# Kernel optimization log

Measured on AMD Instinct MI355X. Metric: run time of the kernel, lower is better.

The kernel has to match this reference:

```python
import jax, jax.numpy as jnp
import numpy as np

B, N, D, H, F = 2, 2048, 512, 8, 2048
HD = D // H
EPS = 1e-5

def _ln(x, g, b):
    m = jnp.mean(x, axis=-1, keepdims=True)
    v = jnp.mean((x - m) ** 2, axis=-1, keepdims=True)
    return (x - m) * jax.lax.rsqrt(v + EPS) * g + b

def setup_inputs() -> dict:
    key = jax.random.key(0)
    ks = jax.random.split(key, 20)
    def lin(k, din, dout, std=0.05):
        kw, kb = jax.random.split(k)
        return (jax.random.normal(kw, (din, dout), jnp.float32) * std,
                jnp.zeros((dout,), jnp.float32))
    Wq, bq = lin(ks[0], D, D)
    Wk, bk = lin(ks[1], D, D)
    Wv, bv = lin(ks[2], D, D)
    Wg, bg = lin(ks[3], D, D)
    Wo, bo = lin(ks[4], D, D)
    W1, b1 = lin(ks[5], D, F)
    W2, b2 = lin(ks[6], F, D)
    return {
        'x': jax.random.normal(ks[7], (B, N, D), jnp.float32),
        'attn_bias': jax.random.normal(ks[8], (B, N, N, H), jnp.float32) * 0.1,
        'attn_mask': jnp.zeros((B, N, N), jnp.bool_),
        'Wq': Wq, 'bq': bq, 'Wk': Wk, 'bk': bk, 'Wv': Wv, 'bv': bv,
        'Wg': Wg, 'bg': bg, 'Wo': Wo, 'bo': bo,
        'ln1_g': jnp.ones((D,), jnp.float32), 'ln1_b': jnp.zeros((D,), jnp.float32),
        'ln2_g': jnp.ones((D,), jnp.float32), 'ln2_b': jnp.zeros((D,), jnp.float32),
        'W1': W1, 'b1': b1, 'W2': W2, 'b2': b2,
    }

def reference(x, attn_bias, attn_mask, Wq, bq, Wk, bk, Wv, bv, Wg, bg, Wo, bo,
              ln1_g, ln1_b, ln2_g, ln2_b, W1, b1, W2, b2):
    scaling = HD ** -0.5
    # --- self-attention sublayer (pre-LN) ---
    y = _ln(x, ln1_g, ln1_b)
    q = (y @ Wq + bq).reshape(B, N, H, HD) * scaling
    k = (y @ Wk + bk).reshape(B, N, H, HD)
    v = (y @ Wv + bv).reshape(B, N, H, HD)
    u = y * jax.nn.sigmoid(y @ Wg + bg)            # GLU gating branch
    scores = jnp.einsum('bqhd,bkhd->bqkh', q, k)   # [B, Nq, Nk, H]
    scores = scores + attn_bias                    # attn_bias_type == 'add'
    scores = jnp.where(attn_mask[..., None], -jnp.inf, scores)
    w = jax.nn.softmax(scores, axis=2)             # softmax over keys
    attn = jnp.einsum('bqkh,bkhd->bqhd', w, v).reshape(B, N, D)
    attn = attn @ Wo + bo
    y = u + attn
    x = x + y                                      # residual (dropout = identity, eval)
    # --- FFN sublayer (pre-LN) ---
    y = _ln(x, ln2_g, ln2_b)
    y = jax.nn.gelu(y @ W1 + b1, approximate=False) @ W2 + b2
    return x + y
```

## Files before the change

### kernel.cpp

```cpp
#include <hip/hip_runtime.h>
#include <hip/hip_bf16.h>

#define DI __device__ __forceinline__

typedef __attribute__((ext_vector_type(8))) __bf16 bf16x8;
typedef __attribute__((ext_vector_type(4))) float f32x4;
typedef __attribute__((ext_vector_type(4))) unsigned short u16x4;
typedef __attribute__((ext_vector_type(8))) unsigned short u16x8;

DI unsigned short f2bs(float f) {
  __hip_bfloat16 h = __float2bfloat16(f);
  return __builtin_bit_cast(unsigned short, h);
}
DI float bs2f(unsigned short s) {
  return __bfloat162float(__builtin_bit_cast(__hip_bfloat16, s));
}
DI f32x4 mfma16(bf16x8 a, bf16x8 b, f32x4 c) {
  return __builtin_amdgcn_mfma_f32_16x16x32_bf16(a, b, c, 0, 0, 0);
}
DI void g2lds16(const void* g, void* l) {
  __builtin_amdgcn_global_load_lds(
      (__attribute__((address_space(1))) void*)(unsigned long long)g,
      (__attribute__((address_space(3))) void*)l, 16, 0, 0);
}
DI void block_sync_lds() {
  asm volatile("s_waitcnt lgkmcnt(0)" ::: "memory");
  __builtin_amdgcn_sched_barrier(0);
  __builtin_amdgcn_s_barrier();
  __builtin_amdgcn_sched_barrier(0);
}

__global__ __launch_bounds__(256) void k_transw(const float* __restrict__ W,
                                                unsigned short* __restrict__ Wt,
                                                int K, int N) {
  __shared__ float tile[64][65];
  int tk = blockIdx.x * 64, tn = blockIdx.y * 64;
  int t = threadIdx.x;
#pragma unroll
  for (int i = 0; i < 16; ++i) {
    int idx = t + i * 256;
    int r = idx >> 6, c = idx & 63;
    tile[r][c] = W[(size_t)(tk + r) * N + tn + c];
  }
  __syncthreads();
#pragma unroll
  for (int i = 0; i < 16; ++i) {
    int idx = t + i * 256;
    int n = idx >> 6, kk = idx & 63;
    Wt[(size_t)(tn + n) * K + tk + kk] = f2bs(tile[kk][n]);
  }
}

__global__ __launch_bounds__(256) void k_bcat(const float* __restrict__ bq,
                                              const float* __restrict__ bk,
                                              const float* __restrict__ bv,
                                              const float* __restrict__ bg,
                                              float* __restrict__ bcat) {
  int t = blockIdx.x * 256 + threadIdx.x;
  const float* src = t < 512 ? bq : t < 1024 ? bk : t < 1536 ? bv : bg;
  bcat[t] = src[t & 511];
}

__global__ __launch_bounds__(256) void k_ln(const float* __restrict__ x,
                                            const float* __restrict__ g,
                                            const float* __restrict__ b,
                                            unsigned short* __restrict__ y) {
  int row = blockIdx.x, t = threadIdx.x;
  const float* xr = x + (size_t)row * 512;
  float a0 = xr[t], a1 = xr[t + 256];
  float s1 = a0 + a1, s2 = a0 * a0 + a1 * a1;
#pragma unroll
  for (int o = 32; o > 0; o >>= 1) {
    s1 += __shfl_down(s1, o);
    s2 += __shfl_down(s2, o);
  }
  __shared__ float r1[4], r2[4], bc[2];
  int w = t >> 6, l = t & 63;
  if (l == 0) { r1[w] = s1; r2[w] = s2; }
  __syncthreads();
  if (t == 0) {
    float t1 = r1[0] + r1[1] + r1[2] + r1[3];
    float t2 = r2[0] + r2[1] + r2[2] + r2[3];
    float m = t1 / 512.f;
    float v = t2 / 512.f - m * m;
    bc[0] = m;
    bc[1] = rsqrtf(v + 1e-5f);
  }
  __syncthreads();
  float m = bc[0], inv = bc[1];
  y[(size_t)row * 512 + t] = f2bs((a0 - m) * inv * g[t] + b[t]);
  y[(size_t)row * 512 + t + 256] = f2bs((a1 - m) * inv * g[t + 256] + b[t + 256]);
}

template <int BM>
__global__ __launch_bounds__(256) void k_gemm(
    const unsigned short* __restrict__ A, const unsigned short* __restrict__ Bt,
    const float* __restrict__ bias, int M, int N, int K, int mode,
    float* __restrict__ outf, unsigned short* __restrict__ outh,
    const float* __restrict__ add1, const float* __restrict__ add2,
    unsigned short* __restrict__ vtout) {
  constexpr int MI = BM / 32;
  __shared__ __align__(16) unsigned short lA[BM * 64];
  __shared__ __align__(16) unsigned short lB[64 * 64];
  int t = threadIdx.x, w = t >> 6, l = t & 63;
  int l15 = l & 15, lg = l >> 4;
  int m0 = blockIdx.x * BM, n0 = blockIdx.y * 64;
  int wm = (w >> 1) * (BM / 2), wn = (w & 1) * 32;
  f32x4 acc[MI][2] = {};
  int sr = l >> 3, scb = (l & 7) * 16;
  for (int k0 = 0; k0 < K; k0 += 64) {
#pragma unroll
    for (int c = 0; c < MI; ++c) {
      int row = w * (BM / 4) + sr + c * 8;
      g2lds16((const char*)A + ((size_t)(m0 + row) * K + k0) * 2 + scb,
              (char*)lA + w * (BM / 4) * 128 + c * 1024);
    }
#pragma unroll
    for (int c = 0; c < 2; ++c) {
      int row = w * 16 + sr + c * 8;
      g2lds16((const char*)Bt + ((size_t)(n0 + row) * K + k0) * 2 + scb,
              (char*)lB + w * 2048 + c * 1024);
    }
    __syncthreads();
#pragma unroll
    for (int kc = 0; kc < 2; ++kc) {
      bf16x8 af[MI], bfr[2];
#pragma unroll
      for (int i = 0; i < MI; ++i)
        af[i] = *(const bf16x8*)((const char*)lA + (wm + i * 16 + l15) * 128 + kc * 64 + lg * 16);
#pragma unroll
      for (int j = 0; j < 2; ++j)
        bfr[j] = *(const bf16x8*)((const char*)lB + (wn + j * 16 + l15) * 128 + kc * 64 + lg * 16);
#pragma unroll
      for (int i = 0; i < MI; ++i)
#pragma unroll
        for (int j = 0; j < 2; ++j)
          acc[i][j] = mfma16(af[i], bfr[j], acc[i][j]);
    }
    __syncthreads();
  }
#pragma unroll
  for (int i = 0; i < MI; ++i) {
#pragma unroll
    for (int j = 0; j < 2; ++j) {
      int col = n0 + wn + j * 16 + l15;
      int row0 = m0 + wm + i * 16 + lg * 4;
      float vals[4];
#pragma unroll
      for (int r = 0; r < 4; ++r) vals[r] = acc[i][j][r] + bias[col];
      if (mode == 6) {
        int sel = col >> 9, c5 = col & 511;
        if (sel == 2) {
          int hh = c5 >> 6, dd = c5 & 63, bb = row0 >> 11, nn = row0 & 2047;
          u16x4 pk;
#pragma unroll
          for (int r = 0; r < 4; ++r) pk[r] = f2bs(vals[r]);
          *(u16x4*)(vtout + (((size_t)(bb * 8 + hh) * 64 + dd) * 2048 + nn)) = pk;
        } else {
#pragma unroll
          for (int r = 0; r < 4; ++r) {
            size_t idx = (size_t)(row0 + r) * 512 + c5;
            if (sel == 0) outh[idx] = f2bs(vals[r] * 0.125f);
            else if (sel == 1) outh[2097152 + idx] = f2bs(vals[r]);
            else outf[idx] = bs2f(A[idx]) * (1.f / (1.f + __expf(-vals[r])));
          }
        }
      } else {
#pragma unroll
        for (int r = 0; r < 4; ++r) {
          size_t idx = (size_t)(row0 + r) * N + col;
          if (mode == 3) outf[idx] = vals[r] + add1[idx] + add2[idx];
          else if (mode == 4) outh[idx] = f2bs(0.5f * vals[r] * (1.f + erff(vals[r] * 0.70710678f)));
          else outf[idx] = vals[r] + add1[idx];
        }
      }
    }
  }
}

__global__ __launch_bounds__(512, 1) void k_attn8(
    const unsigned short* __restrict__ q, const unsigned short* __restrict__ kk,
    const unsigned short* __restrict__ vt, const float* __restrict__ bias,
    const unsigned char* __restrict__ mask, unsigned short* __restrict__ ao) {
  __shared__ __align__(16) unsigned short lsB[2][16 * 260];
  __shared__ __align__(16) unsigned short ls_p[8][16][36];

  int bid = blockIdx.x;
  int b = bid & 1, qt = bid >> 1;
  int q0 = qt * 16;
  int t = threadIdx.x, w = t >> 6, l = t & 63;
  int l15 = l & 15, lg = l >> 4;
  int h = w;

  bf16x8 qa0 = *(const bf16x8*)(q + ((size_t)(b * 2048 + q0 + l15) * 512 + h * 64 + lg * 8));
  bf16x8 qa1 = *(const bf16x8*)(q + ((size_t)(b * 2048 + q0 + l15) * 512 + h * 64 + 32 + lg * 8));

  union { bf16x8 v; unsigned short s[8]; } uo;
#pragma unroll
  for (int j = 0; j < 8; ++j) uo.s[j] = 0x3F80;
  const bf16x8 vones = uo.v;

  f32x4 oacc[4] = {};
  f32x4 lacc = {};

  const unsigned short* kbase = kk + ((size_t)(b * 2048) + l15) * 512 + h * 64 + lg * 8;
  const unsigned short* vbase = vt + ((size_t)(b * 8 + h) * 64 + l15) * 2048 + lg * 8;

  int qq = t >> 5, kc = t & 31;
  const float* bptr = bias + ((size_t)(b * 2048 + q0 + qq) * 2048 + kc) * 8;
  const unsigned char* mptr = mask + (size_t)(b * 2048 + q0 + qq) * 2048 + kc;
  const unsigned short BN = f2bs(-1e30f);

#define LOADB(BA, BB, MB, kb)                                                \
  do {                                                                       \
    BA = *(const float4*)(bptr + (size_t)(kb) * 8);                          \
    BB = *(const float4*)(bptr + (size_t)(kb) * 8 + 4);                      \
    MB = mptr[kb];                                                           \
  } while (0)
#define WRITEB(buf, BA, BB, MB)                                              \
  do {                                                                       \
    u16x4 o0, o1;                                                            \
    if (MB) {                                                                \
      o0[0] = o0[1] = o0[2] = o0[3] = BN;                                    \
      o1[0] = o1[1] = o1[2] = o1[3] = BN;                                    \
    } else {                                                                 \
      o0[0] = f2bs(BA.x); o0[1] = f2bs(BA.y); o0[2] = f2bs(BA.z);            \
      o0[3] = f2bs(BA.w); o1[0] = f2bs(BB.x); o1[1] = f2bs(BB.y);            \
      o1[2] = f2bs(BB.z); o1[3] = f2bs(BB.w);                                \
    }                                                                        \
    *(u16x4*)&lsB[buf][qq * 260 + kc * 8] = o0;                              \
    *(u16x4*)&lsB[buf][qq * 260 + kc * 8 + 4] = o1;                          \
  } while (0)
#define COMPUTE(buf, kb)                                                     \
  do {                                                                       \
    const unsigned short* kp = kbase + (size_t)(kb)*512;                     \
    bf16x8 k00 = *(const bf16x8*)(kp);                                       \
    bf16x8 k01 = *(const bf16x8*)(kp + 32);                                  \
    bf16x8 k10 = *(const bf16x8*)(kp + 16 * 512);                            \
    bf16x8 k11 = *(const bf16x8*)(kp + 16 * 512 + 32);                       \
    const unsigned short* vp = vbase + (kb);                                 \
    bf16x8 v0 = *(const bf16x8*)(vp);                                        \
    bf16x8 v1 = *(const bf16x8*)(vp + 16 * 2048);                            \
    bf16x8 v2 = *(const bf16x8*)(vp + 32 * 2048);                            \
    bf16x8 v3 = *(const bf16x8*)(vp + 48 * 2048);                            \
    f32x4 sc0 = {}, sc1 = {};                                                \
    sc0 = mfma16(qa0, k00, sc0);                                             \
    sc0 = mfma16(qa1, k01, sc0);                                             \
    sc1 = mfma16(qa0, k10, sc1);                                             \
    sc1 = mfma16(qa1, k11, sc1);                                             \
    _Pragma("unroll") for (int r = 0; r < 4; ++r) {                          \
      int qr = lg * 4 + r;                                                   \
      float b0 = bs2f(lsB[buf][qr * 260 + l15 * 8 + h]);                     \
      float b1 = bs2f(lsB[buf][qr * 260 + (l15 + 16) * 8 + h]);              \
      float p0 = __expf(sc0[r] + b0 - 8.0f);                                 \
      float p1 = __expf(sc1[r] + b1 - 8.0f);                                 \
      ls_p[w][qr][l15] = f2bs(p0);                                           \
      ls_p[w][qr][16 + l15] = f2bs(p1);                                      \
    }                                                                        \
    bf16x8 pa = *(const bf16x8*)&ls_p[w][l15][lg * 8];                       \
    oacc[0] = mfma16(pa, v0, oacc[0]);                                       \
    oacc[1] = mfma16(pa, v1, oacc[1]);                                       \
    oacc[2] = mfma16(pa, v2, oacc[2]);                                       \
    oacc[3] = mfma16(pa, v3, oacc[3]);                                       \
    lacc = mfma16(pa, vones, lacc);                                          \
  } while (0)

  float4 bA0, bA1, bB0, bB1;
  unsigned char mA, mB;
  LOADB(bA0, bA1, mA, 0);
  WRITEB(0, bA0, bA1, mA);
  LOADB(bB0, bB1, mB, 32);
  block_sync_lds();
  for (int it = 0; it < 64; it += 2) {
    int kb2 = (it + 2 < 64) ? (it + 2) * 32 : 0;
    LOADB(bA0, bA1, mA, kb2);
    COMPUTE(0, it * 32);
    WRITEB(1, bB0, bB1, mB);
    block_sync_lds();
    int kb3 = (it + 3 < 64) ? (it + 3) * 32 : 0;
    LOADB(bB0, bB1, mB, kb3);
    COMPUTE(1, (it + 1) * 32);
    WRITEB(0, bA0, bA1, mA);
    block_sync_lds();
  }
#undef LOADB
#undef WRITEB
#undef COMPUTE

#pragma unroll
  for (int d = 0; d < 4; ++d)
#pragma unroll
    for (int r = 0; r < 4; ++r) {
      size_t row = (size_t)(b * 2048 + q0 + lg * 4 + r);
      ao[row * 512 + h * 64 + d * 16 + l15] = f2bs(oacc[d][r] / lacc[r]);
    }
}

extern "C" void kernel_launch(void* const* d_in, const int* in_sizes, int n_in,
                              void* d_out, int out_size, void* d_ws, size_t ws_size,
                              hipStream_t stream) {
  (void)in_sizes; (void)n_in; (void)out_size; (void)ws_size;
  const float* x = (const float*)d_in[0];
  const float* abias = (const float*)d_in[1];
  const unsigned char* amask = (const unsigned char*)d_in[2];
  const float* Wq = (const float*)d_in[3];
  const float* bq = (const float*)d_in[4];
  const float* Wk = (const float*)d_in[5];
  const float* bk = (const float*)d_in[6];
  const float* Wv = (const float*)d_in[7];
  const float* bv = (const float*)d_in[8];
  const float* Wg = (const float*)d_in[9];
  const float* bg = (const float*)d_in[10];
  const float* Wo = (const float*)d_in[11];
  const float* bo = (const float*)d_in[12];
  const float* ln1g = (const float*)d_in[13];
  const float* ln1b = (const float*)d_in[14];
  const float* ln2g = (const float*)d_in[15];
  const float* ln2b = (const float*)d_in[16];
  const float* W1 = (const float*)d_in[17];
  const float* b1 = (const float*)d_in[18];
  const float* W2 = (const float*)d_in[19];
  const float* b2 = (const float*)d_in[20];
  float* outp = (float*)d_out;

  char* ws = (char*)d_ws;
  const size_t MB = 1024 * 1024;

  unsigned short* qb = (unsigned short*)(ws + 0);
  unsigned short* kb = (unsigned short*)(ws + 4 * MB);
  unsigned short* ao = (unsigned short*)(ws + 8 * MB);
  unsigned short* y1 = (unsigned short*)(ws + 28 * MB);
  unsigned short* h1 = (unsigned short*)(ws + 0);
  float* u = (float*)(ws + 32 * MB);
  unsigned short* wcat = (unsigned short*)(ws + 40 * MB);
  unsigned short* wot = (unsigned short*)(ws + 42 * MB);
  unsigned short* w1t = (unsigned short*)(ws + 42 * MB + 512 * 1024);
  unsigned short* w2t = (unsigned short*)(ws + 44 * MB + 512 * 1024);
  float* bcat = (float*)(ws + 46 * MB + 512 * 1024);
  unsigned short* vtb = (unsigned short*)(ws + 48 * MB);
  float* x2 = (float*)d_out;

  k_transw<<<dim3(8, 8), 256, 0, stream>>>(Wq, wcat + 0 * 512 * 512, 512, 512);
  k_transw<<<dim3(8, 8), 256, 0, stream>>>(Wk, wcat + 1 * 512 * 512, 512, 512);
  k_transw<<<dim3(8, 8), 256, 0, stream>>>(Wv, wcat + 2 * 512 * 512, 512, 512);
  k_transw<<<dim3(8, 8), 256, 0, stream>>>(Wg, wcat + 3 * 512 * 512, 512, 512);
  k_transw<<<dim3(8, 8), 256, 0, stream>>>(Wo, wot, 512, 512);
  k_transw<<<dim3(8, 32), 256, 0, stream>>>(W1, w1t, 512, 2048);
  k_transw<<<dim3(32, 8), 256, 0, stream>>>(W2, w2t, 2048, 512);
  k_bcat<<<8, 256, 0, stream>>>(bq, bk, bv, bg, bcat);

  k_ln<<<4096, 256, 0, stream>>>(x, ln1g, ln1b, y1);
  k_gemm<128><<<dim3(32, 32), 256, 0, stream>>>(y1, wcat, bcat, 4096, 2048, 512, 6,
                                                u, qb, nullptr, nullptr, vtb);
  k_attn8<<<256, 512, 0, stream>>>(qb, kb, vtb, abias, amask, ao);
  k_gemm<64><<<dim3(64, 8), 256, 0, stream>>>(ao, wot, bo, 4096, 512, 512, 3,
                                              x2, nullptr, u, x, nullptr);
  k_ln<<<4096, 256, 0, stream>>>(x2, ln2g, ln2b, y1);
  k_gemm<128><<<dim3(32, 32), 256, 0, stream>>>(y1, w1t, b1, 4096, 2048, 512, 4,
                                                nullptr, h1, nullptr, nullptr, nullptr);
  k_gemm<64><<<dim3(64, 8), 256, 0, stream>>>(h1, w2t, b2, 4096, 512, 2048, 5,
                                              outp, nullptr, x2, nullptr, nullptr);
}
```

Before: 289.9 us.

## Split attention over key chunks and add a combine kernel

The attention kernel now splits the 2048 keys into 4 chunks. Each block processes one (batch, query tile, key chunk) and writes unnormalized bf16 partial outputs plus fp32 row sums to workspace, so the grid grows from 256 to 1024 blocks. A new combine kernel sums the partials and divides by the summed normalizer, which works because the softmax uses a fixed offset rather than a running max. The aim is more parallelism and occupancy on a 256-CU part while the bias stream is read. The cost is an extra launch, extra partial-output memory traffic, and some rounding from storing partials in bf16.

```diff
diff --git a/kernel.cpp b/kernel.cpp
--- a/kernel.cpp
+++ b/kernel.cpp
@@ -178,16 +178,23 @@
   }
 }
 
-__global__ __launch_bounds__(512, 1) void k_attn8(
+template <int NKS>
+__global__ __launch_bounds__(512, 8) void k_attn9(
     const unsigned short* __restrict__ q, const unsigned short* __restrict__ kk,
     const unsigned short* __restrict__ vt, const float* __restrict__ bias,
-    const unsigned char* __restrict__ mask, unsigned short* __restrict__ ao) {
+    const unsigned char* __restrict__ mask, unsigned short* __restrict__ opart,
+    float* __restrict__ lpart) {
   __shared__ __align__(16) unsigned short lsB[2][16 * 260];
   __shared__ __align__(16) unsigned short ls_p[8][16][36];
 
   int bid = blockIdx.x;
-  int b = bid & 1, qt = bid >> 1;
+  int b = bid & 1;
+  int rest = bid >> 1;
+  int qt = rest & 127;
+  int ksp = rest >> 7;
   int q0 = qt * 16;
+  int kbase0 = ksp * (2048 / NKS);
+  const int ITERS = 2048 / NKS / 32;
   int t = threadIdx.x, w = t >> 6, l = t & 63;
   int l15 = l & 15, lg = l >> 4;
   int h = w;
@@ -267,19 +274,19 @@
 
   float4 bA0, bA1, bB0, bB1;
   unsigned char mA, mB;
-  LOADB(bA0, bA1, mA, 0);
+  LOADB(bA0, bA1, mA, kbase0);
   WRITEB(0, bA0, bA1, mA);
-  LOADB(bB0, bB1, mB, 32);
+  LOADB(bB0, bB1, mB, kbase0 + 32);
   block_sync_lds();
-  for (int it = 0; it < 64; it += 2) {
-    int kb2 = (it + 2 < 64) ? (it + 2) * 32 : 0;
+  for (int it = 0; it < ITERS; it += 2) {
+    int kb2 = (it + 2 < ITERS) ? kbase0 + (it + 2) * 32 : kbase0;
     LOADB(bA0, bA1, mA, kb2);
-    COMPUTE(0, it * 32);
+    COMPUTE(0, kbase0 + it * 32);
     WRITEB(1, bB0, bB1, mB);
     block_sync_lds();
-    int kb3 = (it + 3 < 64) ? (it + 3) * 32 : 0;
+    int kb3 = (it + 3 < ITERS) ? kbase0 + (it + 3) * 32 : kbase0;
     LOADB(bB0, bB1, mB, kb3);
-    COMPUTE(1, (it + 1) * 32);
+    COMPUTE(1, kbase0 + (it + 1) * 32);
     WRITEB(0, bA0, bA1, mA);
     block_sync_lds();
   }
@@ -291,9 +298,33 @@
   for (int d = 0; d < 4; ++d)
 #pragma unroll
     for (int r = 0; r < 4; ++r) {
-      size_t row = (size_t)(b * 2048 + q0 + lg * 4 + r);
-      ao[row * 512 + h * 64 + d * 16 + l15] = f2bs(oacc[d][r] / lacc[r]);
-    }
+      size_t row = (size_t)(ksp * 4096 + b * 2048 + q0 + lg * 4 + r);
+      opart[row * 512 + h * 64 + d * 16 + l15] = f2bs(oacc[d][r]);
+    }
+  if (l15 == 0) {
+#pragma unroll
+    for (int r = 0; r < 4; ++r) {
+      size_t row = (size_t)(ksp * 4096 + b * 2048 + q0 + lg * 4 + r);
+      lpart[row * 8 + h] = lacc[r];
+    }
+  }
+}
+
+template <int NKS>
+__global__ __launch_bounds__(256) void k_comb2(const unsigned short* __restrict__ op,
+                                               const float* __restrict__ lp,
+                                               unsigned short* __restrict__ ao) {
+  int row = blockIdx.x, t = threadIdx.x;
+  for (int c = t; c < 512; c += 256) {
+    int h = c >> 6;
+    float L = 0.f, o = 0.f;
+#pragma unroll
+    for (int s = 0; s < NKS; ++s) {
+      L += lp[(size_t)(s * 4096 + row) * 8 + h];
+      o += bs2f(op[(size_t)(s * 4096 + row) * 512 + c]);
+    }
+    ao[(size_t)row * 512 + c] = f2bs(o / L);
+  }
 }
 
 extern "C" void kernel_launch(void* const* d_in, const int* in_sizes, int n_in,
@@ -329,6 +360,7 @@
   unsigned short* qb = (unsigned short*)(ws + 0);
   unsigned short* kb = (unsigned short*)(ws + 4 * MB);
   unsigned short* ao = (unsigned short*)(ws + 8 * MB);
+  unsigned short* opart = (unsigned short*)(ws + 12 * MB);
   unsigned short* y1 = (unsigned short*)(ws + 28 * MB);
   unsigned short* h1 = (unsigned short*)(ws + 0);
   float* u = (float*)(ws + 32 * MB);
@@ -337,6 +369,7 @@
   unsigned short* w1t = (unsigned short*)(ws + 42 * MB + 512 * 1024);
   unsigned short* w2t = (unsigned short*)(ws + 44 * MB + 512 * 1024);
   float* bcat = (float*)(ws + 46 * MB + 512 * 1024);
+  float* lpart = (float*)(ws + 47 * MB);
   unsigned short* vtb = (unsigned short*)(ws + 48 * MB);
   float* x2 = (float*)d_out;
 
@@ -352,7 +385,8 @@
   k_ln<<<4096, 256, 0, stream>>>(x, ln1g, ln1b, y1);
   k_gemm<128><<<dim3(32, 32), 256, 0, stream>>>(y1, wcat, bcat, 4096, 2048, 512, 6,
                                                 u, qb, nullptr, nullptr, vtb);
-  k_attn8<<<256, 512, 0, stream>>>(qb, kb, vtb, abias, amask, ao);
+  k_attn9<4><<<1024, 512, 0, stream>>>(qb, kb, vtb, abias, amask, opart, lpart);
+  k_comb2<4><<<4096, 256, 0, stream>>>(opart, lpart, ao);
   k_gemm<64><<<dim3(64, 8), 256, 0, stream>>>(ao, wot, bo, 4096, 512, 512, 3,
                                               x2, nullptr, u, x, nullptr);
   k_ln<<<4096, 256, 0, stream>>>(x2, ln2g, ln2b, y1);
```

Result: slower. 460.7 us (+58.9%).

## Halve attention query tile to 8 rows, doubling block count for occupancy

Applied to the files above, without the earlier changes.

The attention kernel now handles 8 query rows per block instead of 16 and is launched with 512 blocks and launch bounds allowing two blocks per CU. The upper half of the bias tile is filled with large negative values so the 16-row MFMA still runs, and only valid rows are written out. Each thread loads half as many bias values per step. The aim is more blocks and more latency hiding on a 256-CU device, at the cost of doing wasted MFMA work on padding rows and reading K/V twice as often.

```diff
diff --git a/kernel.cpp b/kernel.cpp
--- a/kernel.cpp
+++ b/kernel.cpp
@@ -178,7 +178,7 @@
   }
 }
 
-__global__ __launch_bounds__(512, 1) void k_attn8(
+__global__ __launch_bounds__(512, 2) void k_attn10(
     const unsigned short* __restrict__ q, const unsigned short* __restrict__ kk,
     const unsigned short* __restrict__ vt, const float* __restrict__ bias,
     const unsigned char* __restrict__ mask, unsigned short* __restrict__ ao) {
@@ -186,12 +186,19 @@
   __shared__ __align__(16) unsigned short ls_p[8][16][36];
 
   int bid = blockIdx.x;
-  int b = bid & 1, qt = bid >> 1;
-  int q0 = qt * 16;
+  int b = bid & 1;
+  int qt8 = bid >> 1;
+  int q0 = qt8 * 8;
   int t = threadIdx.x, w = t >> 6, l = t & 63;
   int l15 = l & 15, lg = l >> 4;
   int h = w;
 
+  const unsigned short BN = f2bs(-1e30f);
+  for (int i = t; i < 8 * 260; i += 512) {
+    lsB[0][8 * 260 + i] = BN;
+    lsB[1][8 * 260 + i] = BN;
+  }
+
   bf16x8 qa0 = *(const bf16x8*)(q + ((size_t)(b * 2048 + q0 + l15) * 512 + h * 64 + lg * 8));
   bf16x8 qa1 = *(const bf16x8*)(q + ((size_t)(b * 2048 + q0 + l15) * 512 + h * 64 + 32 + lg * 8));
 
@@ -206,30 +213,25 @@
   const unsigned short* kbase = kk + ((size_t)(b * 2048) + l15) * 512 + h * 64 + lg * 8;
   const unsigned short* vbase = vt + ((size_t)(b * 8 + h) * 64 + l15) * 2048 + lg * 8;
 
-  int qq = t >> 5, kc = t & 31;
-  const float* bptr = bias + ((size_t)(b * 2048 + q0 + qq) * 2048 + kc) * 8;
+  int qq = t >> 6, hf = (t >> 5) & 1, kc = t & 31;
+  const float* bptr = bias + ((size_t)(b * 2048 + q0 + qq) * 2048 + kc) * 8 + hf * 4;
   const unsigned char* mptr = mask + (size_t)(b * 2048 + q0 + qq) * 2048 + kc;
-  const unsigned short BN = f2bs(-1e30f);
-
-#define LOADB(BA, BB, MB, kb)                                                \
+
+#define LOADB(BA, MB, kb)                                                    \
   do {                                                                       \
     BA = *(const float4*)(bptr + (size_t)(kb) * 8);                          \
-    BB = *(const float4*)(bptr + (size_t)(kb) * 8 + 4);                      \
     MB = mptr[kb];                                                           \
   } while (0)
-#define WRITEB(buf, BA, BB, MB)                                              \
+#define WRITEB(buf, BA, MB)                                                  \
   do {                                                                       \
-    u16x4 o0, o1;                                                            \
+    u16x4 o0;                                                                \
     if (MB) {                                                                \
       o0[0] = o0[1] = o0[2] = o0[3] = BN;                                    \
-      o1[0] = o1[1] = o1[2] = o1[3] = BN;                                    \
     } else {                                                                 \
-      o0[0] = f2bs(BA.x); o0[1] = f2bs(BA.y); o0[2] = f2bs(BA.z);            \
-      o0[3] = f2bs(BA.w); o1[0] = f2bs(BB.x); o1[1] = f2bs(BB.y);            \
-      o1[2] = f2bs(BB.z); o1[3] = f2bs(BB.w);                                \
+      o0[0] = f2bs(BA.x); o0[1] = f2bs(BA.y);                                \
+      o0[2] = f2bs(BA.z); o0[3] = f2bs(BA.w);                                \
     }                                                                        \
-    *(u16x4*)&lsB[buf][qq * 260 + kc * 8] = o0;                              \
-    *(u16x4*)&lsB[buf][qq * 260 + kc * 8 + 4] = o1;                          \
+    *(u16x4*)&lsB[buf][qq * 260 + kc * 8 + hf * 4] = o0;                     \
   } while (0)
 #define COMPUTE(buf, kb)                                                     \
   do {                                                                       \
@@ -265,35 +267,37 @@
     lacc = mfma16(pa, vones, lacc);                                          \
   } while (0)
 
-  float4 bA0, bA1, bB0, bB1;
+  float4 bA, bB;
   unsigned char mA, mB;
-  LOADB(bA0, bA1, mA, 0);
-  WRITEB(0, bA0, bA1, mA);
-  LOADB(bB0, bB1, mB, 32);
+  LOADB(bA, mA, 0);
+  WRITEB(0, bA, mA);
+  LOADB(bB, mB, 32);
   block_sync_lds();
   for (int it = 0; it < 64; it += 2) {
     int kb2 = (it + 2 < 64) ? (it + 2) * 32 : 0;
-    LOADB(bA0, bA1, mA, kb2);
+    LOADB(bA, mA, kb2);
     COMPUTE(0, it * 32);
-    WRITEB(1, bB0, bB1, mB);
+    WRITEB(1, bB, mB);
     block_sync_lds();
     int kb3 = (it + 3 < 64) ? (it + 3) * 32 : 0;
-    LOADB(bB0, bB1, mB, kb3);
+    LOADB(bB, mB, kb3);
     COMPUTE(1, (it + 1) * 32);
-    WRITEB(0, bA0, bA1, mA);
+    WRITEB(0, bA, mA);
     block_sync_lds();
   }
 #undef LOADB
 #undef WRITEB
 #undef COMPUTE
 
-#pragma unroll
-  for (int d = 0; d < 4; ++d)
-#pragma unroll
-    for (int r = 0; r < 4; ++r) {
-      size_t row = (size_t)(b * 2048 + q0 + lg * 4 + r);
-      ao[row * 512 + h * 64 + d * 16 + l15] = f2bs(oacc[d][r] / lacc[r]);
-    }
+  if (lg < 2) {
+#pragma unroll
+    for (int d = 0; d < 4; ++d)
+#pragma unroll
+      for (int r = 0; r < 4; ++r) {
+        size_t row = (size_t)(b * 2048 + q0 + lg * 4 + r);
+        ao[row * 512 + h * 64 + d * 16 + l15] = f2bs(oacc[d][r] / lacc[r]);
+      }
+  }
 }
 
 extern "C" void kernel_launch(void* const* d_in, const int* in_sizes, int n_in,
@@ -352,7 +356,7 @@
   k_ln<<<4096, 256, 0, stream>>>(x, ln1g, ln1b, y1);
   k_gemm<128><<<dim3(32, 32), 256, 0, stream>>>(y1, wcat, bcat, 4096, 2048, 512, 6,
                                                 u, qb, nullptr, nullptr, vtb);
-  k_attn8<<<256, 512, 0, stream>>>(qb, kb, vtb, abias, amask, ao);
+  k_attn10<<<512, 512, 0, stream>>>(qb, kb, vtb, abias, amask, ao);
   k_gemm<64><<<dim3(64, 8), 256, 0, stream>>>(ao, wot, bo, 4096, 512, 512, 3,
                                               x2, nullptr, u, x, nullptr);
   k_ln<<<4096, 256, 0, stream>>>(x2, ln2g, ln2b, y1);
```

Result: slower. 399.2 us (+37.7%).
